# Optimization experiments

Hardware: AMD Instinct MI355X
Metric: run time of the kernel (lower is better)

Reference implementation:

```python
import jax, jax.numpy as jnp
import numpy as np

N, E, DIM, H = 100000, 1600000, 128, 8
HD = DIM // H


def setup_inputs() -> dict:
    key = jax.random.key(0)
    ks = jax.random.split(key, 12)
    inp = {
        'x': jax.random.normal(ks[0], (N, DIM), dtype=jnp.float32),
        'src': jax.random.randint(ks[1], (E,), 0, N, dtype=jnp.int32),
        'dst': jax.random.randint(ks[2], (E,), 0, N, dtype=jnp.int32),
    }
    scale = 1.0 / np.sqrt(DIM)
    for i, nm in enumerate(['q', 'k', 'v', 'o']):
        inp['W' + nm] = jax.random.normal(ks[3 + 2 * i], (DIM, DIM), dtype=jnp.float32) * scale
        inp['b' + nm] = jax.random.normal(ks[4 + 2 * i], (DIM,), dtype=jnp.float32) * 0.01
    return inp


def reference(x, src, dst, Wq, bq, Wk, bk, Wv, bv, Wo, bo):
    n = x.shape[0]
    q = (x @ Wq + bq).reshape(n, H, HD)
    k = (x @ Wk + bk).reshape(n, H, HD)
    v = (x @ Wv + bv).reshape(n, H, HD)
    # per-edge score: dot(q[src], k[dst]) over head_dim  -> [E, H]
    scores = jnp.einsum('ehd,ehd->eh', q[src], k[dst]) / np.sqrt(HD).astype(np.float32)
    # edge softmax grouped by destination node
    m = jax.ops.segment_max(scores, dst, num_segments=n)        # [N, H]
    e = jnp.exp(scores - m[dst])                                 # [E, H]
    z = jax.ops.segment_sum(e, dst, num_segments=n)              # [N, H]
    attn = e / z[dst]                                            # [E, H]
    # weighted scatter-sum of source values into destinations
    agg = jax.ops.segment_sum(v[src] * attn[:, :, None], dst, num_segments=n)  # [N, H, HD]
    out = agg.reshape(n, DIM) @ Wo + bo
    return out
```

## Files before the change

kernel.cpp:

```cpp
#include <hip/hip_runtime.h>
#include <hip/hip_bf16.h>
#include <math.h>


#define CAP 64
#define CUR_STRIDE 16

typedef __attribute__((ext_vector_type(8))) short short8;
typedef __attribute__((ext_vector_type(4))) float f32x4;

__device__ inline unsigned short f2bf(float f) {
    unsigned u = __float_as_uint(f);
    unsigned r = u + 0x7fffu + ((u >> 16) & 1u);
    return (unsigned short)(r >> 16);
}
__device__ inline float bfhi2f(unsigned u) { return __uint_as_float(u & 0xffff0000u); }
__device__ inline float bflo2f(unsigned u) { return __uint_as_float(u << 16); }

__device__ inline float w_perm(const float* Wq, const float* Wk, const float* Wv,
                               int k, int c) {
    if (c < 256) {
        int g = c >> 2, r = c & 3;
        return (r < 2) ? Wq[k * 128 + 2 * g + r] : Wv[k * 128 + 2 * g + (r - 2)];
    }
    return Wk[k * 128 + (c - 256)];
}

__global__ void pack_b_kernel(const float* __restrict__ Wq, const float* __restrict__ Wk,
                              const float* __restrict__ Wv, const float* __restrict__ Wo,
                              const float* __restrict__ bq, const float* __restrict__ bk,
                              const float* __restrict__ bv,
                              short* __restrict__ BqkvP, short* __restrict__ BoP,
                              float* __restrict__ bqkv) {
    int t = blockIdx.x * 256 + threadIdx.x;
    if (t < 24 * 4 * 64 * 8) {
        int j = t & 7, l = (t >> 3) & 63, ks = (t >> 9) & 3, ct = t >> 11;
        int c = ct * 16 + (l & 15);
        int k = ks * 32 + (l >> 4) * 8 + j;
        BqkvP[t] = (short)f2bf(w_perm(Wq, Wk, Wv, k, c));
    }
    if (t < 8 * 4 * 64 * 8) {
        int j = t & 7, l = (t >> 3) & 63, ks = (t >> 9) & 3, ct = t >> 11;
        int c = ct * 16 + (l & 15);
        int k = ks * 32 + (l >> 4) * 8 + j;
        BoP[t] = (short)f2bf(Wo[k * 128 + c]);
    }
    if (t < 384) {
        float v;
        if (t < 256) {
            int g = t >> 2, r = t & 3;
            v = (r < 2) ? bq[2 * g + r] : bv[2 * g + (r - 2)];
        } else v = bk[t - 256];
        bqkv[t] = v;
    }
}

#define QKV_STRIDE 392
__global__ __launch_bounds__(256) void gemm_qkv_mfma(const float* __restrict__ A,
        const short* __restrict__ Bp, const float* __restrict__ bias,
        short* __restrict__ qv, short* __restrict__ kb, int M) {
    __shared__ short stage[4][16][QKV_STRIDE];
    int w = threadIdx.x >> 6, l = threadIdx.x & 63;
    int row0 = blockIdx.x * 64 + w * 16;
    int lr = l & 15, lk = l >> 4;

    f32x4 acc[24];
    #pragma unroll
    for (int ct = 0; ct < 24; ++ct) {
        float b = bias[ct * 16 + lr];
        acc[ct][0] = b; acc[ct][1] = b; acc[ct][2] = b; acc[ct][3] = b;
    }

    int arow = row0 + lr;
    bool rowok = arow < M;
    const float* arp = A + (size_t)arow * 128;

    #pragma unroll
    for (int ks = 0; ks < 4; ++ks) {
        f32x4 a0 = {0.f, 0.f, 0.f, 0.f}, a1 = {0.f, 0.f, 0.f, 0.f};
        if (rowok) {
            a0 = *(const f32x4*)(arp + ks * 32 + lk * 8);
            a1 = *(const f32x4*)(arp + ks * 32 + lk * 8 + 4);
        }
        short8 af;
        af[0] = (short)f2bf(a0[0]); af[1] = (short)f2bf(a0[1]);
        af[2] = (short)f2bf(a0[2]); af[3] = (short)f2bf(a0[3]);
        af[4] = (short)f2bf(a1[0]); af[5] = (short)f2bf(a1[1]);
        af[6] = (short)f2bf(a1[2]); af[7] = (short)f2bf(a1[3]);
        #pragma unroll
        for (int ct = 0; ct < 24; ++ct) {
            short8 bf = *(const short8*)(Bp + ((size_t)(ct * 4 + ks) * 64 + l) * 8);
            acc[ct] = __builtin_amdgcn_mfma_f32_16x16x32_bf16(af, bf, acc[ct], 0, 0, 0);
        }
    }

    #pragma unroll
    for (int ct = 0; ct < 24; ++ct) {
        int c = ct * 16 + lr;
        #pragma unroll
        for (int j = 0; j < 4; ++j)
            stage[w][lk * 4 + j][c] = (short)f2bf(acc[ct][j]);
    }
    __syncthreads();

    #pragma unroll
    for (int it = 0; it < 8; ++it) {
        int rr = it * 2 + (l >> 5);
        int row = row0 + rr;
        if (row < M) {
            short8 vqv = *(const short8*)&stage[w][rr][(l & 31) * 8];
            *(short8*)(qv + (size_t)row * 256 + (l & 31) * 8) = vqv;
        }
    }
    #pragma unroll
    for (int it = 0; it < 4; ++it) {
        int rr = it * 4 + (l >> 4);
        int row = row0 + rr;
        if (row < M) {
            short8 vk = *(const short8*)&stage[w][rr][256 + (l & 15) * 8];
            *(short8*)(kb + (size_t)row * 128 + (l & 15) * 8) = vk;
        }
    }
}

__global__ __launch_bounds__(256) void gemm_out_mfma(const short* __restrict__ A,
        const short* __restrict__ Bp, const float* __restrict__ bias,
        float* __restrict__ C, int M) {
    int w = threadIdx.x >> 6, l = threadIdx.x & 63;
    int row0 = blockIdx.x * 64 + w * 16;
    int lr = l & 15, lk = l >> 4;

    f32x4 acc[8];
    #pragma unroll
    for (int ct = 0; ct < 8; ++ct) {
        float b = bias[ct * 16 + lr];
        acc[ct][0] = b; acc[ct][1] = b; acc[ct][2] = b; acc[ct][3] = b;
    }

    int arow = row0 + lr;
    bool rowok = arow < M;
    const short* arp = A + (size_t)arow * 128;

    #pragma unroll
    for (int ks = 0; ks < 4; ++ks) {
        short8 af = {0, 0, 0, 0, 0, 0, 0, 0};
        if (rowok) af = *(const short8*)(arp + ks * 32 + lk * 8);
        #pragma unroll
        for (int ct = 0; ct < 8; ++ct) {
            short8 bf = *(const short8*)(Bp + ((size_t)(ct * 4 + ks) * 64 + l) * 8);
            acc[ct] = __builtin_amdgcn_mfma_f32_16x16x32_bf16(af, bf, acc[ct], 0, 0, 0);
        }
    }

    #pragma unroll
    for (int ct = 0; ct < 8; ++ct) {
        int c = ct * 16 + lr;
        #pragma unroll
        for (int j = 0; j < 4; ++j) {
            int r = row0 + lk * 4 + j;
            if (r < M) C[(size_t)r * 128 + c] = acc[ct][j];
        }
    }
}

__global__ void build_kernel(const int* __restrict__ src, const int* __restrict__ dst,
                             int* __restrict__ cursor, int* __restrict__ csr, int E) {
    int e = blockIdx.x * 256 + threadIdx.x;
    if (e < E) {
        int d = dst[e];
        int slot = atomicAdd(&cursor[d << 4], 1);
        if (slot < CAP) csr[((size_t)d << 6) + slot] = src[e];
    }
}

#define EDGE_BODY(ss)                                                          \
    {                                                                          \
        uint2 u = *(const uint2*)(qv + (size_t)(ss) * 256 + l * 4);            \
        float p = bflo2f(u.x) * kdx + bfhi2f(u.x) * kdy;                       \
        p += __shfl_xor(p, 1);                                                 \
        p += __shfl_xor(p, 2);                                                 \
        p += __shfl_xor(p, 4);                                                 \
        float e = __expf(p * 0.25f);                                           \
        z += e;                                                                \
        ax += e * bflo2f(u.y);                                                 \
        ay += e * bfhi2f(u.y);                                                 \
    }

__global__ __launch_bounds__(256) void edge_attn_fused(const short* __restrict__ qv,
        const short* __restrict__ kb, const int* __restrict__ cursor,
        const int* __restrict__ csr, short* __restrict__ agg, int N) {
    int wv = threadIdx.x >> 6;
    int l  = threadIdx.x & 63;
    int d  = blockIdx.x * 4 + wv;
    if (d >= N) return;

    int deg = cursor[d << 4];
    int n = (deg < CAP) ? deg : CAP;
    const int* ep = csr + ((size_t)d << 6);
    unsigned kpk = __builtin_nontemporal_load((const unsigned*)(kb + (size_t)d * 128 + 2 * l));
    float kdx = bflo2f(kpk), kdy = bfhi2f(kpk);

    float z = 0.f, ax = 0.f, ay = 0.f;
    int i = 0;
    for (; i + 4 <= n; i += 4) {
        int s0 = ep[i];
        int s1 = ep[i + 1];
        int s2 = ep[i + 2];
        int s3 = ep[i + 3];
        EDGE_BODY(s0)
        EDGE_BODY(s1)
        EDGE_BODY(s2)
        EDGE_BODY(s3)
    }
    for (; i < n; ++i) {
        int s0 = ep[i];
        EDGE_BODY(s0)
    }

    float zi = (z > 0.f) ? 1.0f / z : 0.f;
    unsigned pk = (unsigned)f2bf(ax * zi) | ((unsigned)f2bf(ay * zi) << 16);
    *(unsigned*)(agg + (size_t)d * 128 + 2 * l) = pk;
}

extern "C" void kernel_launch(void* const* d_in, const int* in_sizes, int n_in,
                              void* d_out, int out_size, void* d_ws, size_t ws_size,
                              hipStream_t stream) {
    const float* x   = (const float*)d_in[0];
    const int*   src = (const int*)d_in[1];
    const int*   dst = (const int*)d_in[2];
    const float* Wq  = (const float*)d_in[3];
    const float* bq  = (const float*)d_in[4];
    const float* Wk  = (const float*)d_in[5];
    const float* bk  = (const float*)d_in[6];
    const float* Wv  = (const float*)d_in[7];
    const float* bv  = (const float*)d_in[8];
    const float* Wo  = (const float*)d_in[9];
    const float* bo  = (const float*)d_in[10];
    float* out = (float*)d_out;

    int N = in_sizes[0] / 128;
    int E = in_sizes[1];

    char* ws = (char*)d_ws;
    size_t off = 0;
    auto alloc = [&](size_t bytes) -> void* {
        void* p = ws + off;
        off = (off + bytes + 255) & ~(size_t)255;
        return p;
    };
    short* BqkvP  = (short*)alloc((size_t)24 * 4 * 64 * 8 * 2);
    short* BoP    = (short*)alloc((size_t)8 * 4 * 64 * 8 * 2);
    float* bqkv   = (float*)alloc(384 * 4);
    short* qv     = (short*)alloc((size_t)N * 256 * 2);
    short* kb     = (short*)alloc((size_t)N * 128 * 2);
    short* agg    = (short*)alloc((size_t)N * 128 * 2);
    int* csr      = (int*)alloc((size_t)N * CAP * 4);
    int* cursor   = (int*)alloc((size_t)N * CUR_STRIDE * 4);
    (void)ws_size; (void)n_in; (void)out_size;

    hipMemsetAsync(cursor, 0, (size_t)N * CUR_STRIDE * 4, stream);

    pack_b_kernel<<<192, 256, 0, stream>>>(Wq, Wk, Wv, Wo, bq, bk, bv, BqkvP, BoP, bqkv);

    gemm_qkv_mfma<<<(N + 63) / 64, 256, 0, stream>>>(x, BqkvP, bqkv, qv, kb, N);

    build_kernel<<<(E + 255) / 256, 256, 0, stream>>>(src, dst, cursor, csr, E);

    edge_attn_fused<<<(N + 3) / 4, 256, 0, stream>>>(qv, kb, cursor, csr, agg, N);

    gemm_out_mfma<<<(N + 63) / 64, 256, 0, stream>>>(agg, BoP, bo, out, N);
}
```

Before: 338.6 us.

## Partition CSR build and edge attention by XCD so destination nodes stay in local L2

Blocks are mapped to XCDs by blockIdx mod 8, and each XCD owns a contiguous eighth of the destination nodes. The build kernel now has each block scan a chunk of edges and apply atomics only for destinations in its XCD's range. The attention kernel processes the same node range on the same XCD. The aim is to keep cursor atomics and the CSR rows in one XCD's L2 and avoid cross-die coherence traffic, at the cost of every edge being read eight times during the build.

```diff
diff --git a/kernel.cpp b/kernel.cpp
--- a/kernel.cpp
+++ b/kernel.cpp
@@ -5,6 +5,7 @@
 
 #define CAP 64
 #define CUR_STRIDE 16
+#define BCHUNK 4096
 
 typedef __attribute__((ext_vector_type(8))) short short8;
 typedef __attribute__((ext_vector_type(4))) float f32x4;
@@ -163,13 +164,24 @@
     }
 }
 
-__global__ void build_kernel(const int* __restrict__ src, const int* __restrict__ dst,
-                             int* __restrict__ cursor, int* __restrict__ csr, int E) {
-    int e = blockIdx.x * 256 + threadIdx.x;
-    if (e < E) {
-        int d = dst[e];
-        int slot = atomicAdd(&cursor[d << 4], 1);
-        if (slot < CAP) csr[((size_t)d << 6) + slot] = src[e];
+__global__ __launch_bounds__(256) void build_kernel(const int* __restrict__ src,
+        const int* __restrict__ dst, int* __restrict__ cursor, int* __restrict__ csr,
+        int E, int per8) {
+    int xcd = blockIdx.x & 7;
+    int chunk = blockIdx.x >> 3;
+    int lo = xcd * per8, hi = lo + per8;
+    int base = chunk * BCHUNK;
+    #pragma unroll
+    for (int it = 0; it < BCHUNK / 256; ++it) {
+        int e = base + it * 256 + threadIdx.x;
+        if (e < E) {
+            int d = dst[e];
+            int s = src[e];
+            if (d >= lo && d < hi) {
+                int slot = atomicAdd(&cursor[d << 4], 1);
+                if (slot < CAP) csr[((size_t)d << 6) + slot] = s;
+            }
+        }
     }
 }
 
@@ -188,10 +200,14 @@
 
 __global__ __launch_bounds__(256) void edge_attn_fused(const short* __restrict__ qv,
         const short* __restrict__ kb, const int* __restrict__ cursor,
-        const int* __restrict__ csr, short* __restrict__ agg, int N) {
+        const int* __restrict__ csr, short* __restrict__ agg, int N, int per8) {
     int wv = threadIdx.x >> 6;
     int l  = threadIdx.x & 63;
-    int d  = blockIdx.x * 4 + wv;
+    int xcd = blockIdx.x & 7;
+    int j   = blockIdx.x >> 3;
+    int local = j * 4 + wv;
+    if (local >= per8) return;
+    int d = xcd * per8 + local;
     if (d >= N) return;
 
     int deg = cursor[d << 4];
@@ -240,6 +256,7 @@
 
     int N = in_sizes[0] / 128;
     int E = in_sizes[1];
+    int per8 = (N + 7) / 8;
 
     char* ws = (char*)d_ws;
     size_t off = 0;
@@ -264,9 +281,11 @@
 
     gemm_qkv_mfma<<<(N + 63) / 64, 256, 0, stream>>>(x, BqkvP, bqkv, qv, kb, N);
 
-    build_kernel<<<(E + 255) / 256, 256, 0, stream>>>(src, dst, cursor, csr, E);
-
-    edge_attn_fused<<<(N + 3) / 4, 256, 0, stream>>>(qv, kb, cursor, csr, agg, N);
+    int nchunks = (E + BCHUNK - 1) / BCHUNK;
+    build_kernel<<<nchunks * 8, 256, 0, stream>>>(src, dst, cursor, csr, E, per8);
+
+    int bpx = (per8 + 3) / 4;
+    edge_attn_fused<<<bpx * 8, 256, 0, stream>>>(qv, kb, cursor, csr, agg, N, per8);
 
     gemm_out_mfma<<<(N + 63) / 64, 256, 0, stream>>>(agg, BoP, bo, out, N);
 }
```

After: 287.8 us. 15.0% less time.
